# Optimization experiments

Hardware: AMD Instinct MI355X
Metric: run time of the kernel (lower is better)

## Reference

```python
import jax, jax.numpy as jnp
import numpy as np

CLASS_NUM = 4            # number of positive classes
NUM_CLASSES = CLASS_NUM + 1  # last column is the negative class
W_P = 4.0
EPS = 1e-9
THR = 0.5


def setup_inputs() -> dict:
    key = jax.random.key(0)
    k1, k2 = jax.random.split(key)
    N = 4_000_000
    x = jax.random.normal(k1, (N, NUM_CLASSES), dtype=jnp.float32)
    t = jax.random.randint(k2, (N,), 0, NUM_CLASSES)
    return {"x": x, "t": t}


def _conf_mpu_loss(x, t):
    N = x.shape[0]
    p = jax.nn.softmax(x, axis=1)                       # [N, C]
    log_pneg = jnp.log(p[:, -1] + EPS)                  # [N]

    ones = jnp.ones((N,), dtype=jnp.float32)
    counts = jax.ops.segment_sum(ones, t, num_segments=NUM_CLASSES)  # per-class counts
    prior = counts[:CLASS_NUM] / N                      # empirical priors (positive classes)

    # loss_per_class: sum over samples with t==c of -log(p[n,c]+eps)
    logp_t = jnp.log(jnp.take_along_axis(p, t[:, None], axis=1)[:, 0] + EPS)
    class_losses = jax.ops.segment_sum(-logp_t, t, num_segments=NUM_CLASSES)

    # loss_per_class_neg: sum over samples with t==i (i positive) of -log(p_neg+eps)
    loss_neg = jax.ops.segment_sum(-log_pneg, t, num_segments=NUM_CLASSES)[:CLASS_NUM]

    # conf_loss_per_class
    conf = []
    for i in range(CLASS_NUM):
        mask = (p[:, i] > THR) & (t == i)
        nsel = jnp.sum(mask.astype(jnp.float32))
        li = jnp.sum(jnp.where(mask, -log_pneg / p[:, i], 0.0))
        conf.append(li / jnp.maximum(nsel, 1.0))        # li==0 when nsel==0
    mask_n = jnp.all(p <= THR, axis=1) & (t == CLASS_NUM)
    li_n = jnp.sum(jnp.where(mask_n, -log_pneg, 0.0))
    conf_neg = li_n / jnp.maximum(counts[CLASS_NUM], 1.0)  # li_n==0 when no selection
    conf_pos = jnp.stack(conf)                          # [CLASS_NUM]

    denom = jnp.maximum(1.0, counts[:CLASS_NUM])
    risk1 = jnp.sum(prior * class_losses[:CLASS_NUM] / denom)
    risk2 = jnp.sum(prior * conf_pos)
    risk3 = jnp.sum(prior * loss_neg / denom)
    risk4 = conf_neg

    positive_risk = W_P * (risk1 + risk2 - risk3)
    positive_risk = jnp.where(positive_risk < 0, 0.0, positive_risk)
    return positive_risk + risk4


def reference(x, t):
    return _conf_mpu_loss(x, t)
```

## Files before the change

### kernel.cpp

```cpp
#include <hip/hip_runtime.h>

namespace {
constexpr int BLOCK = 256;
constexpr float WPF = 4.0f;
constexpr float LN2 = 0.69314718056f;
}

__device__ __forceinline__ float wave_reduce(float v) {
#pragma unroll
    for (int o = 32; o > 0; o >>= 1) v += __shfl_down(v, o, 64);
    return v;
}

__global__ __launch_bounds__(BLOCK) void mpu_main(const float* __restrict__ x,
                                                  const int* __restrict__ t,
                                                  float* __restrict__ acc, int N) {
    __shared__ float red[BLOCK / 64][16];

    float S1 = 0.f, S3 = 0.f, li0 = 0.f, li1 = 0.f, li2 = 0.f, li3 = 0.f, liN = 0.f;
    int c0 = 0, c1 = 0, c2 = 0, c3 = 0, n0 = 0, n1 = 0, n2 = 0, n3 = 0;

    auto process = [&](float x0, float x1, float x2, float x3, float x4, int tc) {
        const float mx = fmaxf(fmaxf(fmaxf(x0, x1), fmaxf(x2, x3)), x4);
        const float e0 = __expf(x0 - mx), e1 = __expf(x1 - mx), e2 = __expf(x2 - mx),
                    e3 = __expf(x3 - mx), e4 = __expf(x4 - mx);
        const float sum = ((e0 + e1) + (e2 + e3)) + e4;
        const float base = fmaf(__log2f(sum), LN2, mx);
        const float nln = base - x4;
        const float xt = (tc == 0) ? x0 : (tc == 1) ? x1 : (tc == 2) ? x2
                       : (tc == 3) ? x3 : x4;
        const float nlt = base - xt;
        const bool tpos = (tc < 4);
        const bool sel = (nlt < LN2);
        const bool alle = (sum >= 2.0f);
        const float confv = sel ? nln * __expf(nlt) : 0.f;

        S1 += tpos ? nlt : 0.f;
        S3 += tpos ? nln : 0.f;
        li0 += (tc == 0) ? confv : 0.f;
        li1 += (tc == 1) ? confv : 0.f;
        li2 += (tc == 2) ? confv : 0.f;
        li3 += (tc == 3) ? confv : 0.f;
        liN += (!tpos && alle) ? nln : 0.f;

        const unsigned long long b0 = __ballot(tc == 0);
        const unsigned long long b1 = __ballot(tc == 1);
        const unsigned long long b2 = __ballot(tc == 2);
        const unsigned long long b3 = __ballot(tc == 3);
        const unsigned long long bs = __ballot(sel);
        c0 += (int)__popcll(b0);
        c1 += (int)__popcll(b1);
        c2 += (int)__popcll(b2);
        c3 += (int)__popcll(b3);
        n0 += (int)__popcll(bs & b0);
        n1 += (int)__popcll(bs & b1);
        n2 += (int)__popcll(bs & b2);
        n3 += (int)__popcll(bs & b3);
    };

    const int pid = blockIdx.x * BLOCK + threadIdx.x;
    const int nOct = N >> 3;

    if (pid < nOct) {
        const float4* xv = reinterpret_cast<const float4*>(x) + (size_t)pid * 10;
        const int4* tv = reinterpret_cast<const int4*>(t) + (size_t)pid * 2;
        const float4 v0 = xv[0], v1 = xv[1], v2 = xv[2], v3 = xv[3], v4 = xv[4];
        const float4 v5 = xv[5], v6 = xv[6], v7 = xv[7], v8 = xv[8], v9 = xv[9];
        const int4 ta = tv[0], tb = tv[1];
        process(v0.x, v0.y, v0.z, v0.w, v1.x, ta.x);
        process(v1.y, v1.z, v1.w, v2.x, v2.y, ta.y);
        process(v2.z, v2.w, v3.x, v3.y, v3.z, ta.z);
        process(v3.w, v4.x, v4.y, v4.z, v4.w, ta.w);
        process(v5.x, v5.y, v5.z, v5.w, v6.x, tb.x);
        process(v6.y, v6.z, v6.w, v7.x, v7.y, tb.y);
        process(v7.z, v7.w, v8.x, v8.y, v8.z, tb.z);
        process(v8.w, v9.x, v9.y, v9.z, v9.w, tb.w);
    }
    if (blockIdx.x == 0 && threadIdx.x == 0) {
        for (int k = (N >> 3) << 3; k < N; ++k)
            process(x[k * 5 + 0], x[k * 5 + 1], x[k * 5 + 2], x[k * 5 + 3],
                    x[k * 5 + 4], t[k]);
    }

    const int wv = threadIdx.x >> 6, ln = threadIdx.x & 63;
    float fr[7] = {S1, S3, li0, li1, li2, li3, liN};
#pragma unroll
    for (int j = 0; j < 7; ++j) {
        const float v = wave_reduce(fr[j]);
        if (ln == 0) red[wv][j] = v;
    }
    if (ln == 0) {
        red[wv][7] = (float)c0;  red[wv][8] = (float)c1;
        red[wv][9] = (float)c2;  red[wv][10] = (float)c3;
        red[wv][11] = (float)n0; red[wv][12] = (float)n1;
        red[wv][13] = (float)n2; red[wv][14] = (float)n3;
    }
    __syncthreads();
    if (threadIdx.x < 15) {
        const float v = red[0][threadIdx.x] + red[1][threadIdx.x] +
                        red[2][threadIdx.x] + red[3][threadIdx.x];
        atomicAdd(&acc[threadIdx.x], v);
    }
}

__global__ void mpu_final(const float* __restrict__ acc, float* __restrict__ out, int N) {
    if (threadIdx.x == 0 && blockIdx.x == 0) {
        const float invN = 1.0f / (float)N;
        const float risk1 = acc[0] * invN;
        const float risk3 = acc[1] * invN;
        float risk2 = 0.0f;
#pragma unroll
        for (int i = 0; i < 4; ++i)
            risk2 += (acc[7 + i] * invN) * (acc[2 + i] / fmaxf(acc[11 + i], 1.0f));
        const float c4 = (float)N - (acc[7] + acc[8] + acc[9] + acc[10]);
        const float risk4 = acc[6] / fmaxf(c4, 1.0f);
        float pos = WPF * (risk1 + risk2 - risk3);
        if (pos < 0.0f) pos = 0.0f;
        out[0] = pos + risk4;
    }
}

extern "C" void kernel_launch(void* const* d_in, const int* in_sizes, int n_in,
                              void* d_out, int out_size, void* d_ws, size_t ws_size,
                              hipStream_t stream) {
    const float* x = (const float*)d_in[0];
    const int* t = (const int*)d_in[1];
    float* out = (float*)d_out;
    float* acc = (float*)d_ws;
    const int N = in_sizes[1];

    hipMemsetAsync(acc, 0, 15 * sizeof(float), stream);

    const int nOct = N >> 3;
    int grid = (nOct + BLOCK - 1) / BLOCK;
    if (grid < 1) grid = 1;
    mpu_main<<<grid, BLOCK, 0, stream>>>(x, t, acc, N);
    mpu_final<<<1, 64, 0, stream>>>(acc, out, N);
}
```

Baseline: 139.1 us.

## Use persistent grid-stride loop with software-prefetched next tile

Caps the grid at 512 blocks and makes each thread loop over multiple 8-row chunks with a grid stride. The next chunk's loads are issued before the current chunk is processed, so memory latency overlaps with compute. This cuts the number of per-block reductions and global atomics, but the two live buffers raise register pressure and the fixed grid may give less memory-level parallelism than one chunk per thread.

```diff
diff --git a/kernel.cpp b/kernel.cpp
--- a/kernel.cpp
+++ b/kernel.cpp
@@ -2,6 +2,7 @@
 
 namespace {
 constexpr int BLOCK = 256;
+constexpr int GRID = 512;
 constexpr float WPF = 4.0f;
 constexpr float LN2 = 0.69314718056f;
 }
@@ -58,24 +59,49 @@
         n3 += (int)__popcll(bs & b3);
     };
 
-    const int pid = blockIdx.x * BLOCK + threadIdx.x;
+    auto load_oct = [&](int g, float4 v[10], int4 t2[2]) {
+        const float4* xv = reinterpret_cast<const float4*>(x) + (size_t)g * 10;
+        const int4* tv = reinterpret_cast<const int4*>(t) + (size_t)g * 2;
+#pragma unroll
+        for (int j = 0; j < 10; ++j) v[j] = xv[j];
+        t2[0] = tv[0];
+        t2[1] = tv[1];
+    };
+
+    auto process8 = [&](const float4 v[10], const int4 t2[2]) {
+        process(v[0].x, v[0].y, v[0].z, v[0].w, v[1].x, t2[0].x);
+        process(v[1].y, v[1].z, v[1].w, v[2].x, v[2].y, t2[0].y);
+        process(v[2].z, v[2].w, v[3].x, v[3].y, v[3].z, t2[0].z);
+        process(v[3].w, v[4].x, v[4].y, v[4].z, v[4].w, t2[0].w);
+        process(v[5].x, v[5].y, v[5].z, v[5].w, v[6].x, t2[1].x);
+        process(v[6].y, v[6].z, v[6].w, v[7].x, v[7].y, t2[1].y);
+        process(v[7].z, v[7].w, v[8].x, v[8].y, v[8].z, t2[1].z);
+        process(v[8].w, v[9].x, v[9].y, v[9].z, v[9].w, t2[1].w);
+    };
+
+    const int stride = gridDim.x * BLOCK;
     const int nOct = N >> 3;
 
-    if (pid < nOct) {
-        const float4* xv = reinterpret_cast<const float4*>(x) + (size_t)pid * 10;
-        const int4* tv = reinterpret_cast<const int4*>(t) + (size_t)pid * 2;
-        const float4 v0 = xv[0], v1 = xv[1], v2 = xv[2], v3 = xv[3], v4 = xv[4];
-        const float4 v5 = xv[5], v6 = xv[6], v7 = xv[7], v8 = xv[8], v9 = xv[9];
-        const int4 ta = tv[0], tb = tv[1];
-        process(v0.x, v0.y, v0.z, v0.w, v1.x, ta.x);
-        process(v1.y, v1.z, v1.w, v2.x, v2.y, ta.y);
-        process(v2.z, v2.w, v3.x, v3.y, v3.z, ta.z);
-        process(v3.w, v4.x, v4.y, v4.z, v4.w, ta.w);
-        process(v5.x, v5.y, v5.z, v5.w, v6.x, tb.x);
-        process(v6.y, v6.z, v6.w, v7.x, v7.y, tb.y);
-        process(v7.z, v7.w, v8.x, v8.y, v8.z, tb.z);
-        process(v8.w, v9.x, v9.y, v9.z, v9.w, tb.w);
+    int g = blockIdx.x * BLOCK + threadIdx.x;
+    float4 cv[10];
+    int4 ct[2];
+    bool have = (g < nOct);
+    if (have) load_oct(g, cv, ct);
+    while (have) {
+        const int gn = g + stride;
+        const bool haveN = (gn < nOct);
+        float4 nv[10];
+        int4 nt2[2];
+        if (haveN) load_oct(gn, nv, nt2);
+        process8(cv, ct);
+#pragma unroll
+        for (int j = 0; j < 10; ++j) cv[j] = nv[j];
+        ct[0] = nt2[0];
+        ct[1] = nt2[1];
+        g = gn;
+        have = haveN;
     }
+
     if (blockIdx.x == 0 && threadIdx.x == 0) {
         for (int k = (N >> 3) << 3; k < N; ++k)
             process(x[k * 5 + 0], x[k * 5 + 1], x[k * 5 + 2], x[k * 5 + 3],
@@ -133,6 +159,7 @@
 
     const int nOct = N >> 3;
     int grid = (nOct + BLOCK - 1) / BLOCK;
+    if (grid > GRID) grid = GRID;
     if (grid < 1) grid = 1;
     mpu_main<<<grid, BLOCK, 0, stream>>>(x, t, acc, N);
     mpu_final<<<1, 64, 0, stream>>>(acc, out, N);
```

Result: no change. 138.3 us (-0.6%).

## Compute softmax terms in log2 domain without max shift and fuse finalize via last-block counter

Applied to the files above, without the earlier changes.

Rewrites per-row math to work in base-2 using exp2 and log intrinsics directly, dropping the max-subtraction and merging the two positive-class sums into one accumulator, with ln2 scaling deferred to the final combine. The separate finalize kernel is removed; the last block to finish, detected with an atomic counter, computes the output. This cuts ALU work per row and one kernel launch, at the cost of possible overflow for very large logits since the max shift is gone.

```diff
diff --git a/kernel.cpp b/kernel.cpp
--- a/kernel.cpp
+++ b/kernel.cpp
@@ -3,7 +3,8 @@
 namespace {
 constexpr int BLOCK = 256;
 constexpr float WPF = 4.0f;
-constexpr float LN2 = 0.69314718056f;
+constexpr float LN2 = 0.69314718055994531f;
+constexpr float LOG2E = 1.44269504088896340f;
 }
 
 __device__ __forceinline__ float wave_reduce(float v) {
@@ -14,34 +15,40 @@
 
 __global__ __launch_bounds__(BLOCK) void mpu_main(const float* __restrict__ x,
                                                   const int* __restrict__ t,
-                                                  float* __restrict__ acc, int N) {
+                                                  float* __restrict__ acc,
+                                                  float* __restrict__ out,
+                                                  int N, int nblk) {
     __shared__ float red[BLOCK / 64][16];
 
-    float S1 = 0.f, S3 = 0.f, li0 = 0.f, li1 = 0.f, li2 = 0.f, li3 = 0.f, liN = 0.f;
+    float S13 = 0.f, li0 = 0.f, li1 = 0.f, li2 = 0.f, li3 = 0.f, liN = 0.f;
     int c0 = 0, c1 = 0, c2 = 0, c3 = 0, n0 = 0, n1 = 0, n2 = 0, n3 = 0;
 
     auto process = [&](float x0, float x1, float x2, float x3, float x4, int tc) {
-        const float mx = fmaxf(fmaxf(fmaxf(x0, x1), fmaxf(x2, x3)), x4);
-        const float e0 = __expf(x0 - mx), e1 = __expf(x1 - mx), e2 = __expf(x2 - mx),
-                    e3 = __expf(x3 - mx), e4 = __expf(x4 - mx);
-        const float sum = ((e0 + e1) + (e2 + e3)) + e4;
-        const float base = fmaf(__log2f(sum), LN2, mx);
-        const float nln = base - x4;
-        const float xt = (tc == 0) ? x0 : (tc == 1) ? x1 : (tc == 2) ? x2
-                       : (tc == 3) ? x3 : x4;
-        const float nlt = base - xt;
+        const float y0 = x0 * LOG2E, y1 = x1 * LOG2E, y2 = x2 * LOG2E,
+                    y3 = x3 * LOG2E, y4 = x4 * LOG2E;
+        const float f0 = __builtin_amdgcn_exp2f(y0);
+        const float f1 = __builtin_amdgcn_exp2f(y1);
+        const float f2 = __builtin_amdgcn_exp2f(y2);
+        const float f3 = __builtin_amdgcn_exp2f(y3);
+        const float f4 = __builtin_amdgcn_exp2f(y4);
+        const float s = ((f0 + f1) + (f2 + f3)) + f4;
+        const float L2 = __builtin_amdgcn_logf(s);
+        const float thr = L2 - 1.0f;
+        const float ymax = fmaxf(fmaxf(fmaxf(y0, y1), fmaxf(y2, y3)), y4);
+        const float yt = (tc == 0) ? y0 : (tc == 1) ? y1 : (tc == 2) ? y2
+                       : (tc == 3) ? y3 : y4;
+        const float nltY = L2 - yt;
+        const float nlnY = L2 - y4;
+        const bool sel = (yt > thr);
+        const bool alle = (ymax <= thr);
         const bool tpos = (tc < 4);
-        const bool sel = (nlt < LN2);
-        const bool alle = (sum >= 2.0f);
-        const float confv = sel ? nln * __expf(nlt) : 0.f;
-
-        S1 += tpos ? nlt : 0.f;
-        S3 += tpos ? nln : 0.f;
-        li0 += (tc == 0) ? confv : 0.f;
-        li1 += (tc == 1) ? confv : 0.f;
-        li2 += (tc == 2) ? confv : 0.f;
-        li3 += (tc == 3) ? confv : 0.f;
-        liN += (!tpos && alle) ? nln : 0.f;
+        S13 += tpos ? (nltY - nlnY) : 0.f;
+        const float cv = sel ? nlnY * __builtin_amdgcn_exp2f(nltY) : 0.f;
+        li0 += (tc == 0) ? cv : 0.f;
+        li1 += (tc == 1) ? cv : 0.f;
+        li2 += (tc == 2) ? cv : 0.f;
+        li3 += (tc == 3) ? cv : 0.f;
+        liN += (tc == 4 && alle) ? nlnY : 0.f;
 
         const unsigned long long b0 = __ballot(tc == 0);
         const unsigned long long b1 = __ballot(tc == 1);
@@ -83,40 +90,45 @@
     }
 
     const int wv = threadIdx.x >> 6, ln = threadIdx.x & 63;
-    float fr[7] = {S1, S3, li0, li1, li2, li3, liN};
+    float fr[6] = {S13, li0, li1, li2, li3, liN};
 #pragma unroll
-    for (int j = 0; j < 7; ++j) {
+    for (int j = 0; j < 6; ++j) {
         const float v = wave_reduce(fr[j]);
         if (ln == 0) red[wv][j] = v;
     }
     if (ln == 0) {
-        red[wv][7] = (float)c0;  red[wv][8] = (float)c1;
-        red[wv][9] = (float)c2;  red[wv][10] = (float)c3;
-        red[wv][11] = (float)n0; red[wv][12] = (float)n1;
-        red[wv][13] = (float)n2; red[wv][14] = (float)n3;
+        red[wv][6] = (float)c0;   red[wv][7] = (float)c1;
+        red[wv][8] = (float)c2;   red[wv][9] = (float)c3;
+        red[wv][10] = (float)n0;  red[wv][11] = (float)n1;
+        red[wv][12] = (float)n2;  red[wv][13] = (float)n3;
     }
     __syncthreads();
-    if (threadIdx.x < 15) {
+    if (threadIdx.x < 14) {
         const float v = red[0][threadIdx.x] + red[1][threadIdx.x] +
                         red[2][threadIdx.x] + red[3][threadIdx.x];
         atomicAdd(&acc[threadIdx.x], v);
     }
-}
+    __syncthreads();
 
-__global__ void mpu_final(const float* __restrict__ acc, float* __restrict__ out, int N) {
-    if (threadIdx.x == 0 && blockIdx.x == 0) {
-        const float invN = 1.0f / (float)N;
-        const float risk1 = acc[0] * invN;
-        const float risk3 = acc[1] * invN;
-        float risk2 = 0.0f;
+    if (threadIdx.x == 0) {
+        __threadfence();
+        const unsigned old = atomicAdd((unsigned*)(acc + 14), 1u);
+        if (old == (unsigned)nblk - 1u) {
+            float a[14];
 #pragma unroll
-        for (int i = 0; i < 4; ++i)
-            risk2 += (acc[7 + i] * invN) * (acc[2 + i] / fmaxf(acc[11 + i], 1.0f));
-        const float c4 = (float)N - (acc[7] + acc[8] + acc[9] + acc[10]);
-        const float risk4 = acc[6] / fmaxf(c4, 1.0f);
-        float pos = WPF * (risk1 + risk2 - risk3);
-        if (pos < 0.0f) pos = 0.0f;
-        out[0] = pos + risk4;
+            for (int i = 0; i < 14; ++i) a[i] = atomicAdd(&acc[i], 0.0f);
+            const float invN = 1.0f / (float)N;
+            const float risk13 = LN2 * a[0] * invN;
+            float risk2 = 0.0f;
+#pragma unroll
+            for (int c = 0; c < 4; ++c)
+                risk2 += (a[6 + c] * invN) * (LN2 * a[1 + c] / fmaxf(a[10 + c], 1.0f));
+            const float c4 = (float)N - (a[6] + a[7] + a[8] + a[9]);
+            const float risk4 = LN2 * a[5] / fmaxf(c4, 1.0f);
+            float pos = WPF * (risk13 + risk2);
+            if (pos < 0.0f) pos = 0.0f;
+            out[0] = pos + risk4;
+        }
     }
 }
 
@@ -129,11 +141,10 @@
     float* acc = (float*)d_ws;
     const int N = in_sizes[1];
 
-    hipMemsetAsync(acc, 0, 15 * sizeof(float), stream);
+    hipMemsetAsync(acc, 0, 64, stream);
 
     const int nOct = N >> 3;
     int grid = (nOct + BLOCK - 1) / BLOCK;
     if (grid < 1) grid = 1;
-    mpu_main<<<grid, BLOCK, 0, stream>>>(x, t, acc, N);
-    mpu_final<<<1, 64, 0, stream>>>(acc, out, N);
+    mpu_main<<<grid, BLOCK, 0, stream>>>(x, t, acc, out, N, grid);
 }
```

Result: slower. 216.2 us (+55.4%).
